# Optimization experiments

Measured on AMD Instinct MI355X. Metric: run time of the kernel, lower is better.

The kernel has to match this reference:

```python
import jax, jax.numpy as jnp
import numpy as np

N_NODES = 50000
N_EDGES = 800000
D = 256
N_LAYERS = 3
BN_EPS = 1e-5


def setup_inputs() -> dict:
    key = jax.random.key(0)
    ks = jax.random.split(key, 7)
    x = jax.random.normal(ks[0], (N_NODES, D), dtype=jnp.float32)
    Wl = jax.random.normal(ks[1], (N_LAYERS, D, D), dtype=jnp.float32)
    bl = jax.random.normal(ks[2], (N_LAYERS, D), dtype=jnp.float32)
    Wr = jax.random.normal(ks[3], (N_LAYERS, D, D), dtype=jnp.float32)
    gamma = jax.random.uniform(ks[4], (N_LAYERS, D), dtype=jnp.float32)
    beta = jax.random.normal(ks[5], (N_LAYERS, D), dtype=jnp.float32)
    edge_index = jax.random.randint(ks[6], (2, N_EDGES), 0, N_NODES, dtype=jnp.int64)
    return {"x": x, "Wl": Wl, "bl": bl, "Wr": Wr, "gamma": gamma,
            "beta": beta, "edge_index": edge_index}


def reference(x, Wl, bl, Wr, gamma, beta, edge_index):
    """3-layer GNN: SAGEConv(mean) -> BatchNorm1d(train) -> ReLU per layer."""
    src = edge_index[0]
    dst = edge_index[1]
    n = x.shape[0]
    # In-degree (mean-aggregation denominator); clamp to avoid div-by-zero.
    deg = jax.ops.segment_sum(jnp.ones((src.shape[0],), dtype=x.dtype), dst,
                              num_segments=n)
    deg = jnp.maximum(deg, 1.0)[:, None]  # [N, 1]
    n_layers = Wl.shape[0]
    for i in range(n_layers):
        # --- SAGEConv: mean-aggregate neighbor messages, then linear ---
        agg = jax.ops.segment_sum(x[src], dst, num_segments=n) / deg  # [N, D]
        h = agg @ Wl[i] + bl[i] + x @ Wr[i]                           # [N, D]
        # --- BatchNorm1d (training mode: batch stats, biased variance) ---
        mu = jnp.mean(h, axis=0)
        var = jnp.mean(jnp.square(h - mu), axis=0)
        h = (h - mu) * jax.lax.rsqrt(var + BN_EPS) * gamma[i] + beta[i]
        # --- ReLU ---
        x = jax.nn.relu(h)
    return x
```

## Files before the change

### kernel.cpp

```cpp
#include <hip/hip_runtime.h>

#define N_NODES 50000
#define N_PAD   50176
#define N_EDGES 800000
#define DIM     256
#define KDIM    512
#define BN_EPS  1e-5f
#define SCAN_NB ((N_NODES + 1023) / 1024)
#define NT      (KDIM / 64)

typedef __attribute__((ext_vector_type(8))) short short8;
typedef __attribute__((ext_vector_type(4))) float floatx4;

__device__ __forceinline__ float bf2f(unsigned short u) {
    return __uint_as_float(((unsigned int)u) << 16);
}
__device__ __forceinline__ unsigned short f2bf(float f) {
    unsigned int b = __float_as_uint(f);
    b = (b + 0x7FFF + ((b >> 16) & 1)) >> 16;
    return (unsigned short)b;
}

__device__ __forceinline__ void gload_lds16(const void* g, void* l) {
    __builtin_amdgcn_global_load_lds(
        (const __attribute__((address_space(1))) unsigned int*)g,
        (__attribute__((address_space(3))) unsigned int*)l, 16, 0, 0);
}


__global__ void k_deg_count(const int* __restrict__ dst, int* __restrict__ degi) {
    int e = blockIdx.x * blockDim.x + threadIdx.x;
    if (e < N_EDGES) atomicAdd(&degi[dst[e]], 1);
}

__global__ void k_scan1(const int* __restrict__ degi, int* __restrict__ off,
                        float* __restrict__ inv_deg, int* __restrict__ bsums) {
    __shared__ int buf[1024];
    int i = blockIdx.x * 1024 + threadIdx.x;
    int v = (i < N_NODES) ? degi[i] : 0;
    if (i < N_NODES) inv_deg[i] = 1.0f / (float)max(v, 1);
    buf[threadIdx.x] = v;
    __syncthreads();
    for (int s = 1; s < 1024; s <<= 1) {
        int t = (threadIdx.x >= s) ? buf[threadIdx.x - s] : 0;
        __syncthreads();
        buf[threadIdx.x] += t;
        __syncthreads();
    }
    if (i < N_NODES) off[i + 1] = buf[threadIdx.x];
    if (threadIdx.x == 1023) bsums[blockIdx.x] = buf[1023];
    if (i == 0) off[0] = 0;
}

__global__ void k_scan3(int* __restrict__ off, const int* __restrict__ bsums) {
    __shared__ int boff;
    int t = threadIdx.x;
    if (t < 64) {
        int v = (t < SCAN_NB && t < (int)blockIdx.x) ? bsums[t] : 0;
        for (int s = 32; s >= 1; s >>= 1) v += __shfl_xor(v, s, 64);
        if (t == 0) boff = v;
    }
    __syncthreads();
    int i = blockIdx.x * 1024 + threadIdx.x;
    if (i < N_NODES) off[i + 1] += boff;
}

__global__ void k_fill(const int* __restrict__ src, const int* __restrict__ dst,
                       const int* __restrict__ off, int* __restrict__ cursor,
                       int* __restrict__ csr_src) {
    int e = blockIdx.x * blockDim.x + threadIdx.x;
    if (e < N_EDGES) {
        int d = dst[e];
        int pos = atomicAdd(&cursor[d], 1);
        csr_src[off[d] + pos] = src[e];
    }
}


#define PREPW_N (3 * DIM * KDIM)
#define X2BF_N  (N_NODES * (DIM / 4))

__global__ void k_prep(const float* __restrict__ Wl, const float* __restrict__ Wr,
                       unsigned short* __restrict__ Wcat,
                       const float* __restrict__ x, unsigned short* __restrict__ Acat) {
    int gid = blockIdx.x * blockDim.x + threadIdx.x;
    if (gid < PREPW_N) {
        int k = gid & (KDIM - 1);
        int n = (gid >> 9) & (DIM - 1);
        int l = gid >> 17;
        float v = (k < DIM) ? Wl[(size_t)l * DIM * DIM + (size_t)k * DIM + n]
                            : Wr[(size_t)l * DIM * DIM + (size_t)(k - DIM) * DIM + n];
        Wcat[gid] = f2bf(v);
        return;
    }
    int xid = gid - PREPW_N;
    if (xid < X2BF_N) {
        int node = xid >> 6;
        int c = (xid & 63) * 4;
        float4 v = ((const float4*)x)[xid];
        ushort4 o; o.x = f2bf(v.x); o.y = f2bf(v.y); o.z = f2bf(v.z); o.w = f2bf(v.w);
        *(ushort4*)&Acat[(size_t)node * KDIM + DIM + c] = o;
    }
}


__device__ __forceinline__ void addv(float* a, uint4 v) {
    unsigned int w[4] = {v.x, v.y, v.z, v.w};
    #pragma unroll
    for (int q = 0; q < 4; ++q) {
        a[2 * q + 0] += bf2f((unsigned short)(w[q] & 0xFFFF));
        a[2 * q + 1] += bf2f((unsigned short)(w[q] >> 16));
    }
}

__global__ __launch_bounds__(256, 8) void k_aggregate(
        const unsigned short* __restrict__ Acat_x,
        const int* __restrict__ off,
        const int* __restrict__ csr_src,
        const float* __restrict__ inv_deg,
        unsigned short* __restrict__ Acat_agg) {
    int gid = blockIdx.x * blockDim.x + threadIdx.x;
    int node = gid >> 5;
    int lane = threadIdx.x & 31;
    if (node >= N_NODES) return;
    int beg = off[node], end = off[node + 1];
    float a[8];
    #pragma unroll
    for (int q = 0; q < 8; ++q) a[q] = 0.f;
    const unsigned short* xb = Acat_x + DIM + lane * 8;

    int e = beg;
    for (; e + 8 <= end; e += 8) {
        uint4 v0 = *(const uint4*)(xb + (size_t)csr_src[e + 0] * KDIM);
        uint4 v1 = *(const uint4*)(xb + (size_t)csr_src[e + 1] * KDIM);
        uint4 v2 = *(const uint4*)(xb + (size_t)csr_src[e + 2] * KDIM);
        uint4 v3 = *(const uint4*)(xb + (size_t)csr_src[e + 3] * KDIM);
        uint4 v4 = *(const uint4*)(xb + (size_t)csr_src[e + 4] * KDIM);
        uint4 v5 = *(const uint4*)(xb + (size_t)csr_src[e + 5] * KDIM);
        uint4 v6 = *(const uint4*)(xb + (size_t)csr_src[e + 6] * KDIM);
        uint4 v7 = *(const uint4*)(xb + (size_t)csr_src[e + 7] * KDIM);
        addv(a, v0); addv(a, v1); addv(a, v2); addv(a, v3);
        addv(a, v4); addv(a, v5); addv(a, v6); addv(a, v7);
    }
    for (; e + 4 <= end; e += 4) {
        uint4 v0 = *(const uint4*)(xb + (size_t)csr_src[e + 0] * KDIM);
        uint4 v1 = *(const uint4*)(xb + (size_t)csr_src[e + 1] * KDIM);
        uint4 v2 = *(const uint4*)(xb + (size_t)csr_src[e + 2] * KDIM);
        uint4 v3 = *(const uint4*)(xb + (size_t)csr_src[e + 3] * KDIM);
        addv(a, v0); addv(a, v1); addv(a, v2); addv(a, v3);
    }
    for (; e < end; ++e) {
        uint4 v = *(const uint4*)(xb + (size_t)csr_src[e] * KDIM);
        addv(a, v);
    }

    float inv = inv_deg[node];
    unsigned int w[4];
    #pragma unroll
    for (int q = 0; q < 4; ++q)
        w[q] = (unsigned int)f2bf(a[2 * q] * inv) |
               ((unsigned int)f2bf(a[2 * q + 1] * inv) << 16);
    uint4 o; o.x = w[0]; o.y = w[1]; o.z = w[2]; o.w = w[3];
    *(uint4*)&Acat_agg[(size_t)node * KDIM + lane * 8] = o;
}


__global__ __launch_bounds__(256) void k_gemm_mfma(
        const unsigned short* __restrict__ A,
        const unsigned short* __restrict__ Bt,
        const float* __restrict__ bias, unsigned short* __restrict__ H,
        float* __restrict__ ssum, float* __restrict__ ssq) {
    __shared__ __align__(16) short Alds[128 * 64];
    __shared__ __align__(16) short Blds[128 * 64];
    int tid = threadIdx.x;
    int wid = tid >> 6;
    int lane = tid & 63;
    int wm = wid >> 1, wn = wid & 1;
    int brow = blockIdx.x * 128;
    int bcol = blockIdx.y * 128;

    floatx4 acc[4][4];
    #pragma unroll
    for (int i = 0; i < 4; ++i)
        #pragma unroll
        for (int j = 0; j < 4; ++j) acc[i][j] = (floatx4){0.f, 0.f, 0.f, 0.f};

    int st_row = lane >> 3;
    int st_s   = lane & 7;
    int sg_st  = st_s ^ st_row;
    int rb = lane & 15;
    int k16r = lane >> 4;

    for (int kt = 0; kt < NT; ++kt) {
        int k0 = kt * 64;
        #pragma unroll
        for (int q = 0; q < 4; ++q) {
            int c = wid * 4 + q;
            int r = c * 8 + st_row;
            gload_lds16(A + (size_t)(brow + r) * KDIM + k0 + sg_st * 8,
                        &Alds[c * 512]);
            gload_lds16(Bt + (size_t)(bcol + r) * KDIM + k0 + sg_st * 8,
                        &Blds[c * 512]);
        }
        __syncthreads();

        #pragma unroll
        for (int kk = 0; kk < 2; ++kk) {
            short8 af[4], bfr[4];
            #pragma unroll
            for (int i = 0; i < 4; ++i) {
                int ra = wm * 64 + i * 16 + rb;
                int s_st = (kk * 4 + k16r) ^ (rb & 7);
                af[i] = *(const short8*)&Alds[ra * 64 + s_st * 8];
                int rc = wn * 64 + i * 16 + rb;
                bfr[i] = *(const short8*)&Blds[rc * 64 + s_st * 8];
            }
            #pragma unroll
            for (int i = 0; i < 4; ++i)
                #pragma unroll
                for (int j = 0; j < 4; ++j)
                    acc[i][j] = __builtin_amdgcn_mfma_f32_16x16x32_bf16(
                        af[i], bfr[j], acc[i][j], 0, 0, 0);
        }
        __syncthreads();
    }

    int rg = lane >> 4;
    #pragma unroll
    for (int j = 0; j < 4; ++j) {
        int col = bcol + wn * 64 + j * 16 + rb;
        float bv = bias[col];
        float s = 0.f, s2 = 0.f;
        #pragma unroll
        for (int i = 0; i < 4; ++i) {
            #pragma unroll
            for (int q = 0; q < 4; ++q) {
                int row = brow + wm * 64 + i * 16 + rg * 4 + q;
                float o = acc[i][j][q] + bv;
                unsigned short hb = f2bf(o);
                if (row < N_NODES) {
                    H[(size_t)row * DIM + col] = hb;
                    float of = bf2f(hb);
                    s += of;
                    s2 = fmaf(of, of, s2);
                }
            }
        }
        s  += __shfl_xor(s, 16);
        s  += __shfl_xor(s, 32);
        s2 += __shfl_xor(s2, 16);
        s2 += __shfl_xor(s2, 32);
        if (rg == 0) {
            atomicAdd(&ssum[col], s);
            atomicAdd(&ssq[col], s2);
        }
    }
}


__global__ void k_norm(const unsigned short* __restrict__ H,
                       const float* __restrict__ ssum, const float* __restrict__ ssq,
                       const float* __restrict__ gamma, const float* __restrict__ beta,
                       unsigned short* __restrict__ Acat) {
    __shared__ float sc[DIM], sh[DIM];
    {
        int c = threadIdx.x;
        float mu  = ssum[c] * (1.0f / N_NODES);
        float var = ssq[c] * (1.0f / N_NODES) - mu * mu;
        float rstd = rsqrtf(var + BN_EPS);
        float s = rstd * gamma[c];
        sc[c] = s;
        sh[c] = beta[c] - mu * s;
    }
    __syncthreads();
    size_t total8 = (size_t)N_NODES * DIM / 8;
    for (size_t i = (size_t)blockIdx.x * blockDim.x + threadIdx.x; i < total8;
         i += (size_t)gridDim.x * blockDim.x) {
        uint4 raw = ((const uint4*)H)[i];
        int node = (int)(i >> 5);
        int c = ((int)i & 31) * 8;
        unsigned int w[4] = {raw.x, raw.y, raw.z, raw.w};
        unsigned int uw[4];
        #pragma unroll
        for (int q = 0; q < 4; ++q) {
            float lo = bf2f((unsigned short)(w[q] & 0xFFFF));
            float hi = bf2f((unsigned short)(w[q] >> 16));
            lo = fmaxf(fmaf(lo, sc[c + q * 2 + 0], sh[c + q * 2 + 0]), 0.f);
            hi = fmaxf(fmaf(hi, sc[c + q * 2 + 1], sh[c + q * 2 + 1]), 0.f);
            uw[q] = (unsigned int)f2bf(lo) | ((unsigned int)f2bf(hi) << 16);
        }
        uint4 u; u.x = uw[0]; u.y = uw[1]; u.z = uw[2]; u.w = uw[3];
        *(uint4*)&Acat[(size_t)node * KDIM + DIM + c] = u;
    }
}


__global__ void k_out(const unsigned short* __restrict__ H,
                      const float* __restrict__ ssum, const float* __restrict__ ssq,
                      const float* __restrict__ gamma, const float* __restrict__ beta,
                      float* __restrict__ outF) {
    __shared__ float sc[DIM], sh[DIM];
    {
        int c = threadIdx.x;
        float mu  = ssum[c] * (1.0f / N_NODES);
        float var = ssq[c] * (1.0f / N_NODES) - mu * mu;
        float rstd = rsqrtf(var + BN_EPS);
        float s = rstd * gamma[c];
        sc[c] = s;
        sh[c] = beta[c] - mu * s;
    }
    __syncthreads();
    size_t total8 = (size_t)N_NODES * DIM / 8;
    for (size_t i = (size_t)blockIdx.x * blockDim.x + threadIdx.x; i < total8;
         i += (size_t)gridDim.x * blockDim.x) {
        uint4 raw = ((const uint4*)H)[i];
        int node = (int)(i >> 5);
        int c = ((int)i & 31) * 8;
        unsigned int w[4] = {raw.x, raw.y, raw.z, raw.w};
        float o[8];
        #pragma unroll
        for (int q = 0; q < 4; ++q) {
            float lo = bf2f((unsigned short)(w[q] & 0xFFFF));
            float hi = bf2f((unsigned short)(w[q] >> 16));
            o[q * 2 + 0] = fmaxf(fmaf(lo, sc[c + q * 2 + 0], sh[c + q * 2 + 0]), 0.f);
            o[q * 2 + 1] = fmaxf(fmaf(hi, sc[c + q * 2 + 1], sh[c + q * 2 + 1]), 0.f);
        }
        float4 f0 = make_float4(o[0], o[1], o[2], o[3]);
        float4 f1 = make_float4(o[4], o[5], o[6], o[7]);
        *(float4*)(outF + (size_t)node * DIM + c)     = f0;
        *(float4*)(outF + (size_t)node * DIM + c + 4) = f1;
    }
}


extern "C" void kernel_launch(void* const* d_in, const int* in_sizes, int n_in,
                              void* d_out, int out_size, void* d_ws, size_t ws_size,
                              hipStream_t stream) {
    const float* x0    = (const float*)d_in[0];
    const float* Wl    = (const float*)d_in[1];
    const float* bl    = (const float*)d_in[2];
    const float* Wr    = (const float*)d_in[3];
    const float* gamma = (const float*)d_in[4];
    const float* beta  = (const float*)d_in[5];
    const int*   ei    = (const int*)d_in[6];
    const int* e_src = ei;
    const int* e_dst = ei + N_EDGES;

    char* ws = (char*)d_ws;
    size_t off = 0;
    auto alloc = [&](size_t bytes) { char* p = ws + off; off = (off + bytes + 255) & ~(size_t)255; return p; };
    unsigned short* Acat = (unsigned short*)alloc((size_t)N_PAD * KDIM * 2);
    unsigned short* Hbuf = (unsigned short*)alloc((size_t)N_PAD * DIM * 2);
    unsigned short* Wcat = (unsigned short*)alloc((size_t)3 * DIM * KDIM * 2);
    int*   csr_src = (int*)alloc((size_t)N_EDGES * 4);
    int*   csr_off = (int*)alloc((size_t)(N_NODES + 1) * 4);
    char*  zbase   = alloc((size_t)50176 * 4 * 2 + 6144);
    int*   degi    = (int*)zbase;
    int*   cursor  = (int*)(zbase + 50176 * 4);
    float* stats   = (float*)(zbase + 50176 * 4 * 2);
    int*   bsums   = (int*)alloc((size_t)SCAN_NB * 4);
    float* inv_deg = (float*)alloc((size_t)N_NODES * 4);
    (void)ws_size;

    hipMemsetAsync(zbase, 0, (size_t)50176 * 4 * 2 + 6144, stream);

    int eb = (N_EDGES + 255) / 256;
    k_deg_count<<<eb, 256, 0, stream>>>(e_dst, degi);
    k_scan1<<<SCAN_NB, 1024, 0, stream>>>(degi, csr_off, inv_deg, bsums);
    k_scan3<<<SCAN_NB, 1024, 0, stream>>>(csr_off, bsums);
    k_fill<<<eb, 256, 0, stream>>>(e_src, e_dst, csr_off, cursor, csr_src);
    k_prep<<<(PREPW_N + X2BF_N + 255) / 256, 256, 0, stream>>>(Wl, Wr, Wcat, x0, Acat);

    int ab = (N_NODES * 32 + 255) / 256;
    for (int l = 0; l < 3; ++l) {
        float* ssum_l = stats + (size_t)l * 2 * DIM;
        float* ssq_l  = ssum_l + DIM;
        k_aggregate<<<ab, 256, 0, stream>>>(Acat, csr_off, csr_src, inv_deg, Acat);
        k_gemm_mfma<<<dim3(N_PAD / 128, DIM / 128), 256, 0, stream>>>(
            Acat, Wcat + (size_t)l * DIM * KDIM, bl + (size_t)l * DIM, Hbuf,
            ssum_l, ssq_l);
        if (l < 2)
            k_norm<<<2048, 256, 0, stream>>>(Hbuf, ssum_l, ssq_l,
                                             gamma + (size_t)l * DIM,
                                             beta + (size_t)l * DIM, Acat);
    }
    float* ssum2 = stats + (size_t)2 * 2 * DIM;
    k_out<<<2048, 256, 0, stream>>>(Hbuf, ssum2, ssum2 + DIM,
                                    gamma + 2 * DIM, beta + 2 * DIM, (float*)d_out);
}
```

Baseline: 703.3 us.

## Restructure GEMM to load full-K A tile once and stream B from global

The GEMM now gives each block 64 rows across all 256 output columns. The whole 64x512 A tile is loaded into LDS once, and B fragments are read straight from global memory, which is expected to hit cache. This removes the per-K-step LDS staging, the repeated barriers and the duplicate reads of A across two column blocks. In exchange it uses 64KB of LDS per block, which lowers occupancy, and adds uncoalesced global reads of B inside the inner loop. It also drops the launch bounds hint on the aggregate kernel.

```diff
diff --git a/kernel.cpp b/kernel.cpp
--- a/kernel.cpp
+++ b/kernel.cpp
@@ -7,7 +7,6 @@
 #define KDIM    512
 #define BN_EPS  1e-5f
 #define SCAN_NB ((N_NODES + 1023) / 1024)
-#define NT      (KDIM / 64)
 
 typedef __attribute__((ext_vector_type(8))) short short8;
 typedef __attribute__((ext_vector_type(4))) float floatx4;
@@ -113,7 +112,7 @@
     }
 }
 
-__global__ __launch_bounds__(256, 8) void k_aggregate(
+__global__ void k_aggregate(
         const unsigned short* __restrict__ Acat_x,
         const int* __restrict__ off,
         const int* __restrict__ csr_src,
@@ -170,72 +169,59 @@
         const unsigned short* __restrict__ Bt,
         const float* __restrict__ bias, unsigned short* __restrict__ H,
         float* __restrict__ ssum, float* __restrict__ ssq) {
-    __shared__ __align__(16) short Alds[128 * 64];
-    __shared__ __align__(16) short Blds[128 * 64];
+    __shared__ __align__(16) short Alds[64 * 512];
     int tid = threadIdx.x;
     int wid = tid >> 6;
     int lane = tid & 63;
     int wm = wid >> 1, wn = wid & 1;
-    int brow = blockIdx.x * 128;
-    int bcol = blockIdx.y * 128;
-
-    floatx4 acc[4][4];
-    #pragma unroll
-    for (int i = 0; i < 4; ++i)
-        #pragma unroll
-        for (int j = 0; j < 4; ++j) acc[i][j] = (floatx4){0.f, 0.f, 0.f, 0.f};
-
-    int st_row = lane >> 3;
-    int st_s   = lane & 7;
-    int sg_st  = st_s ^ st_row;
+    int brow = blockIdx.x * 64;
+
+    #pragma unroll
+    for (int i = 0; i < 16; ++i) {
+        int L = i * 256 + tid;
+        int r = L >> 6;
+        int s = L & 63;
+        int sg = s ^ r;
+        gload_lds16(A + (size_t)(brow + r) * KDIM + sg * 8, &Alds[(size_t)L * 8]);
+    }
+    __syncthreads();
+
     int rb = lane & 15;
-    int k16r = lane >> 4;
-
-    for (int kt = 0; kt < NT; ++kt) {
-        int k0 = kt * 64;
-        #pragma unroll
-        for (int q = 0; q < 4; ++q) {
-            int c = wid * 4 + q;
-            int r = c * 8 + st_row;
-            gload_lds16(A + (size_t)(brow + r) * KDIM + k0 + sg_st * 8,
-                        &Alds[c * 512]);
-            gload_lds16(Bt + (size_t)(bcol + r) * KDIM + k0 + sg_st * 8,
-                        &Blds[c * 512]);
-        }
-        __syncthreads();
-
-        #pragma unroll
-        for (int kk = 0; kk < 2; ++kk) {
-            short8 af[4], bfr[4];
-            #pragma unroll
-            for (int i = 0; i < 4; ++i) {
-                int ra = wm * 64 + i * 16 + rb;
-                int s_st = (kk * 4 + k16r) ^ (rb & 7);
-                af[i] = *(const short8*)&Alds[ra * 64 + s_st * 8];
-                int rc = wn * 64 + i * 16 + rb;
-                bfr[i] = *(const short8*)&Blds[rc * 64 + s_st * 8];
-            }
-            #pragma unroll
-            for (int i = 0; i < 4; ++i)
-                #pragma unroll
-                for (int j = 0; j < 4; ++j)
-                    acc[i][j] = __builtin_amdgcn_mfma_f32_16x16x32_bf16(
-                        af[i], bfr[j], acc[i][j], 0, 0, 0);
-        }
-        __syncthreads();
-    }
-
     int rg = lane >> 4;
-    #pragma unroll
-    for (int j = 0; j < 4; ++j) {
-        int col = bcol + wn * 64 + j * 16 + rb;
+
+    floatx4 acc[2][8];
+    #pragma unroll
+    for (int i = 0; i < 2; ++i)
+        #pragma unroll
+        for (int j = 0; j < 8; ++j) acc[i][j] = (floatx4){0.f, 0.f, 0.f, 0.f};
+
+    for (int kt = 0; kt < KDIM / 32; ++kt) {
+        short8 af[2];
+        #pragma unroll
+        for (int i = 0; i < 2; ++i) {
+            int r = wm * 32 + i * 16 + rb;
+            int slot = (kt * 4 + rg) ^ r;
+            af[i] = *(const short8*)&Alds[r * 512 + slot * 8];
+        }
+        #pragma unroll
+        for (int j = 0; j < 8; ++j) {
+            int c = wn * 128 + j * 16 + rb;
+            short8 bf = *(const short8*)&Bt[(size_t)c * KDIM + kt * 32 + rg * 8];
+            acc[0][j] = __builtin_amdgcn_mfma_f32_16x16x32_bf16(af[0], bf, acc[0][j], 0, 0, 0);
+            acc[1][j] = __builtin_amdgcn_mfma_f32_16x16x32_bf16(af[1], bf, acc[1][j], 0, 0, 0);
+        }
+    }
+
+    #pragma unroll
+    for (int j = 0; j < 8; ++j) {
+        int col = wn * 128 + j * 16 + rb;
         float bv = bias[col];
         float s = 0.f, s2 = 0.f;
         #pragma unroll
-        for (int i = 0; i < 4; ++i) {
+        for (int i = 0; i < 2; ++i) {
             #pragma unroll
             for (int q = 0; q < 4; ++q) {
-                int row = brow + wm * 64 + i * 16 + rg * 4 + q;
+                int row = brow + wm * 32 + i * 16 + rg * 4 + q;
                 float o = acc[i][j][q] + bv;
                 unsigned short hb = f2bf(o);
                 if (row < N_NODES) {
@@ -376,7 +362,7 @@
         float* ssum_l = stats + (size_t)l * 2 * DIM;
         float* ssq_l  = ssum_l + DIM;
         k_aggregate<<<ab, 256, 0, stream>>>(Acat, csr_off, csr_src, inv_deg, Acat);
-        k_gemm_mfma<<<dim3(N_PAD / 128, DIM / 128), 256, 0, stream>>>(
+        k_gemm_mfma<<<N_PAD / 64, 256, 0, stream>>>(
             Acat, Wcat + (size_t)l * DIM * KDIM, bl + (size_t)l * DIM, Hbuf,
             ssum_l, ssq_l);
         if (l < 2)
```

Measured after the change: 746.5 us. 6.1% more time.
